# Kernel tuning notes

Hardware: AMD Instinct MI355X
Metric: run time of the kernel (lower is better)

The kernel has to match this reference:

```python
import jax, jax.numpy as jnp
import numpy as np

B, S, E = 4, 2048, 1024

def setup_inputs() -> dict:
    key = jax.random.key(0)
    ks = jax.random.split(key, 9)
    lim = 1.0 / np.sqrt(E)
    inp = {
        "query": jax.random.normal(ks[0], (B, S, E), dtype=jnp.float32),
        "key": jax.random.normal(ks[1], (B, S, E), dtype=jnp.float32),
        "value": jax.random.normal(ks[2], (B, S, E), dtype=jnp.float32),
        "Wq": jax.random.uniform(ks[3], (E, E), jnp.float32, -lim, lim),
        "bq": jax.random.uniform(ks[4], (E,), jnp.float32, -lim, lim),
        "Wk": jax.random.uniform(ks[5], (E, E), jnp.float32, -lim, lim),
        "bk": jax.random.uniform(ks[6], (E,), jnp.float32, -lim, lim),
        "Wv": jax.random.uniform(ks[7], (E, E), jnp.float32, -lim, lim),
        "bv": jax.random.uniform(ks[8], (E,), jnp.float32, -lim, lim),
    }
    return inp

def reference(query, key, value, Wq, bq, Wk, bk, Wv, bv):
    # Linear layers (torch stores weight as [out,in]; here W is [in,out] used as x @ W)
    q = query @ Wq + bq            # [B,S,E]
    k = key @ Wk + bk              # [B,S,E]
    v = value @ Wv + bv            # [B,S,E]
    inv_scale = jnp.asarray(E, q.dtype) ** 0.5
    scores = jnp.einsum("bse,bte->bst", q, k) / inv_scale  # [B,S,S]
    attn = jax.nn.softmax(scores, axis=-1)
    # dropout_p = 0.0 -> identity
    out = jnp.einsum("bst,bte->bse", attn, v)  # [B,S,E]
    return out
```

## Files before the change

### kernel.cpp

```cpp
#include <hip/hip_runtime.h>
#include <hip/hip_bf16.h>


typedef __bf16 bf16_t;
typedef bf16_t bf16x8 __attribute__((ext_vector_type(8)));
typedef bf16_t bf16x4 __attribute__((ext_vector_type(4)));
typedef float  f32x4  __attribute__((ext_vector_type(4)));

typedef const __attribute__((address_space(1))) unsigned gl_uint;
typedef __attribute__((address_space(3))) unsigned lds_uint;

#define BM 128
#define BN 128
#define BK 64

__device__ __forceinline__ void gload_lds16(const bf16_t* g, bf16_t* l) {
  __builtin_amdgcn_global_load_lds((gl_uint*)g, (lds_uint*)l, 16, 0, 0);
}

__device__ __forceinline__ void gemm_core(
    const bf16_t* __restrict__ Ab, const bf16_t* __restrict__ Bb,
    const int K, bf16_t* As, bf16_t* Bs, f32x4 acc[4][4])
{
  const int tid  = threadIdx.x;
  const int lane = tid & 63;
  const int quad = lane >> 4;
  const int l15  = lane & 15;
  const int wid  = tid >> 6;
  const int wm   = (wid >> 1) * 64;
  const int wn   = (wid & 1) * 64;
  const int csw  = l15 & 7;

  for (int kt = 0; kt < K; kt += BK) {
#pragma unroll
    for (int j = 0; j < 4; ++j) {
      const int lin = j * 256 + tid;
      const int row = lin >> 3;
      const int seg = (lin & 7) ^ (row & 7);
      gload_lds16(Ab + (size_t)row * K + kt + seg * 8, &As[lin * 8]);
    }
#pragma unroll
    for (int j = 0; j < 4; ++j) {
      const int lin = j * 256 + tid;
      const int row = lin >> 3;
      const int seg = (lin & 7) ^ (row & 7);
      gload_lds16(Bb + (size_t)row * K + kt + seg * 8, &Bs[lin * 8]);
    }
    __syncthreads();

#pragma unroll
    for (int ks = 0; ks < 2; ++ks) {
      const int sg = ks * 4 + quad;
      const int c  = (sg ^ csw) * 8;
      bf16x8 fa[4], fb[4];
#pragma unroll
      for (int i = 0; i < 4; ++i)
        fa[i] = *(const bf16x8*)&As[(wm + i * 16 + l15) * BK + c];
#pragma unroll
      for (int i = 0; i < 4; ++i)
        fb[i] = *(const bf16x8*)&Bs[(wn + i * 16 + l15) * BK + c];
#pragma unroll
      for (int mi = 0; mi < 4; ++mi)
#pragma unroll
        for (int ni = 0; ni < 4; ++ni)
          acc[mi][ni] = __builtin_amdgcn_mfma_f32_16x16x32_bf16(
              fa[mi], fb[ni], acc[mi][ni], 0, 0, 0);
    }
    __syncthreads();
  }
}

__global__ __launch_bounds__(256, 2)
void qkv_proj(const bf16_t* __restrict__ qb, const bf16_t* __restrict__ kb,
              const bf16_t* __restrict__ vb, const bf16_t* __restrict__ Wqt,
              const bf16_t* __restrict__ Wkt, const bf16_t* __restrict__ Wvt,
              const float* __restrict__ bq, const float* __restrict__ bk,
              const float* __restrict__ bv, bf16_t* __restrict__ qp,
              bf16_t* __restrict__ kp, bf16_t* __restrict__ vT)
{
  __shared__ __align__(16) bf16_t As[BM * BK];
  __shared__ __align__(16) bf16_t Bs[BN * BK];
  const int z = blockIdx.z;
  const bf16_t* A = (z == 0) ? qb : (z == 1) ? kb : vb;
  const bf16_t* W = (z == 0) ? Wqt : (z == 1) ? Wkt : Wvt;
  const float* bias = (z == 0) ? bq : (z == 1) ? bk : bv;

  const int K = 1024, N = 1024;
  const bf16_t* Ab = A + (size_t)blockIdx.y * BM * K;
  const bf16_t* Bb = W + (size_t)blockIdx.x * BN * K;

  f32x4 acc[4][4];
  const f32x4 z4 = {0.f, 0.f, 0.f, 0.f};
#pragma unroll
  for (int i = 0; i < 4; ++i)
#pragma unroll
    for (int j = 0; j < 4; ++j) acc[i][j] = z4;

  gemm_core(Ab, Bb, K, As, Bs, acc);

  const int lane = threadIdx.x & 63;
  const int quad = lane >> 4;
  const int l15  = lane & 15;
  const int wid  = threadIdx.x >> 6;
  const int wm = (wid >> 1) * 64, wn = (wid & 1) * 64;
  const int m0 = blockIdx.y * BM, n0 = blockIdx.x * BN;

#pragma unroll
  for (int mi = 0; mi < 4; ++mi) {
#pragma unroll
    for (int ni = 0; ni < 4; ++ni) {
      const int gn = n0 + wn + ni * 16 + l15;
      const int gm = m0 + wm + mi * 16 + quad * 4;
      const float bv_ = bias[gn];
      f32x4 a = acc[mi][ni];
      if (z < 2) {
        bf16_t* C = (z == 0) ? qp : kp;
#pragma unroll
        for (int r = 0; r < 4; ++r)
          C[(size_t)(gm + r) * N + gn] = (bf16_t)(a[r] + bv_);
      } else {
        const int b = gm >> 11;
        const int s = gm & 2047;
        bf16x4 o;
#pragma unroll
        for (int r = 0; r < 4; ++r) o[r] = (bf16_t)(a[r] + bv_);
        *(bf16x4*)&vT[((size_t)b * N + gn) * 2048 + s] = o;
      }
    }
  }
}

template <int MODE>
__global__ __launch_bounds__(256, 2)
void gemm_att(const bf16_t* __restrict__ A, const bf16_t* __restrict__ Bt,
              void* __restrict__ Cv, float* __restrict__ lsum,
              const int M, const int N, const int K,
              const long long sA, const long long sB, const long long sC)
{
  __shared__ __align__(16) bf16_t As[BM * BK];
  __shared__ __align__(16) bf16_t Bs[BN * BK];
  const int bz = blockIdx.z;
  const bf16_t* Ab = A + (size_t)bz * sA + (size_t)blockIdx.y * BM * K;
  const bf16_t* Bb = Bt + (size_t)bz * sB + (size_t)blockIdx.x * BN * K;

  f32x4 acc[4][4];
  const f32x4 z4 = {0.f, 0.f, 0.f, 0.f};
#pragma unroll
  for (int i = 0; i < 4; ++i)
#pragma unroll
    for (int j = 0; j < 4; ++j) acc[i][j] = z4;

  gemm_core(Ab, Bb, K, As, Bs, acc);

  const int lane = threadIdx.x & 63;
  const int quad = lane >> 4;
  const int l15  = lane & 15;
  const int wid  = threadIdx.x >> 6;
  const int wm = (wid >> 1) * 64, wn = (wid & 1) * 64;
  const int m0 = blockIdx.y * BM, n0 = blockIdx.x * BN;

  if (MODE == 0) {
    const float cexp = 0.03125f * 1.4426950408889634f;
    bf16_t* C = (bf16_t*)Cv + (size_t)bz * sC;
    float* lrow = lsum + (size_t)bz * M;
#pragma unroll
    for (int mi = 0; mi < 4; ++mi) {
      const int gm = m0 + wm + mi * 16 + quad * 4;
      float ps[4] = {0.f, 0.f, 0.f, 0.f};
#pragma unroll
      for (int ni = 0; ni < 4; ++ni) {
        const int gn = n0 + wn + ni * 16 + l15;
        f32x4 a = acc[mi][ni];
        float e[4];
#pragma unroll
        for (int r = 0; r < 4; ++r) {
          e[r] = exp2f(a[r] * cexp);
          C[(size_t)(gm + r) * N + gn] = (bf16_t)e[r];
          ps[r] += e[r];
        }
      }
#pragma unroll
      for (int o = 1; o <= 8; o <<= 1)
#pragma unroll
        for (int r = 0; r < 4; ++r) ps[r] += __shfl_xor(ps[r], o);
      if (l15 == 0) {
#pragma unroll
        for (int r = 0; r < 4; ++r) atomicAdd(&lrow[gm + r], ps[r]);
      }
    }
  } else {
    float* C = (float*)Cv + (size_t)bz * sC;
    const float* lrow = lsum + (size_t)bz * M;
#pragma unroll
    for (int mi = 0; mi < 4; ++mi) {
      const int gm = m0 + wm + mi * 16 + quad * 4;
      float il[4];
#pragma unroll
      for (int r = 0; r < 4; ++r) il[r] = 1.0f / lrow[gm + r];
#pragma unroll
      for (int ni = 0; ni < 4; ++ni) {
        const int gn = n0 + wn + ni * 16 + l15;
        f32x4 a = acc[mi][ni];
#pragma unroll
        for (int r = 0; r < 4; ++r)
          C[(size_t)(gm + r) * N + gn] = a[r] * il[r];
      }
    }
  }
}

__global__ __launch_bounds__(256)
void cvt3_k(const float* __restrict__ q, const float* __restrict__ k,
            const float* __restrict__ v, bf16_t* __restrict__ qo,
            bf16_t* __restrict__ ko, bf16_t* __restrict__ vo) {
  const int z = blockIdx.y;
  const float* in = (z == 0) ? q : (z == 1) ? k : v;
  bf16_t* out = (z == 0) ? qo : (z == 1) ? ko : vo;
  const size_t i = ((size_t)blockIdx.x * 256 + threadIdx.x) * 4;
  const float4 w = *(const float4*)(in + i);
  bf16x4 o;
  o[0] = (bf16_t)w.x; o[1] = (bf16_t)w.y; o[2] = (bf16_t)w.z; o[3] = (bf16_t)w.w;
  *(bf16x4*)(out + i) = o;
}

__global__ __launch_bounds__(256)
void transpose_cvt3(const float* __restrict__ Wq, const float* __restrict__ Wk,
                    const float* __restrict__ Wv, bf16_t* __restrict__ Wqt,
                    bf16_t* __restrict__ Wkt, bf16_t* __restrict__ Wvt) {
  const int z = blockIdx.z;
  const float* W = (z == 0) ? Wq : (z == 1) ? Wk : Wv;
  bf16_t* Wt = (z == 0) ? Wqt : (z == 1) ? Wkt : Wvt;
  __shared__ float tile[64][65];
  const int n0 = blockIdx.x * 64;
  const int k0 = blockIdx.y * 64;
  const int tid = threadIdx.x;
#pragma unroll
  for (int it = 0; it < 16; ++it) {
    const int idx = it * 256 + tid;
    const int r = idx >> 6, c = idx & 63;
    tile[r][c] = W[(size_t)(k0 + r) * 1024 + n0 + c];
  }
  __syncthreads();
#pragma unroll
  for (int it = 0; it < 16; ++it) {
    const int idx = it * 256 + tid;
    const int r = idx >> 6, c = idx & 63;
    Wt[(size_t)(n0 + r) * 1024 + k0 + c] = (bf16_t)tile[c][r];
  }
}

extern "C" void kernel_launch(void* const* d_in, const int* in_sizes, int n_in,
                              void* d_out, int out_size, void* d_ws, size_t ws_size,
                              hipStream_t stream) {
  const int B = 4, S = 2048, E = 1024;
  const size_t BSE = (size_t)B * S * E;
  const size_t EE  = (size_t)E * E;

  const float* q_in = (const float*)d_in[0];
  const float* k_in = (const float*)d_in[1];
  const float* v_in = (const float*)d_in[2];
  const float* Wq = (const float*)d_in[3];
  const float* bq = (const float*)d_in[4];
  const float* Wk = (const float*)d_in[5];
  const float* bk = (const float*)d_in[6];
  const float* Wv = (const float*)d_in[7];
  const float* bv = (const float*)d_in[8];
  float* out = (float*)d_out;

  char* ws = (char*)d_ws;
  bf16_t* qb  = (bf16_t*)ws;
  bf16_t* kb  = qb + BSE;
  bf16_t* vb  = kb + BSE;
  bf16_t* Wqt = vb + BSE;
  bf16_t* Wkt = Wqt + EE;
  bf16_t* Wvt = Wkt + EE;
  bf16_t* qp  = Wvt + EE;
  bf16_t* kp  = qp + BSE;
  bf16_t* vT  = kp + BSE;
  bf16_t* P   = vT + BSE;
  float*  lsum = (float*)(P + (size_t)B * S * S);

  cvt3_k<<<dim3(BSE / 1024, 3), 256, 0, stream>>>(q_in, k_in, v_in, qb, kb, vb);
  transpose_cvt3<<<dim3(16, 16, 3), 256, 0, stream>>>(Wq, Wk, Wv, Wqt, Wkt, Wvt);
  hipMemsetAsync(lsum, 0, (size_t)B * S * sizeof(float), stream);

  qkv_proj<<<dim3(E / BN, (B * S) / BM, 3), 256, 0, stream>>>(
      qb, kb, vb, Wqt, Wkt, Wvt, bq, bk, bv, qp, kp, vT);

  gemm_att<0><<<dim3(S / BN, S / BM, B), 256, 0, stream>>>(
      qp, kp, P, lsum, S, S, E,
      (long long)S * E, (long long)S * E, (long long)S * S);

  gemm_att<1><<<dim3(E / BN, S / BM, B), 256, 0, stream>>>(
      P, vT, out, lsum, S, E, S,
      (long long)S * S, (long long)E * S, (long long)S * E);

  (void)in_sizes; (void)n_in; (void)out_size; (void)ws_size;
}
```

Baseline: 319.6 us.

## Fuse fp32-to-bf16 input conversion into QKV GEMM and remap blocks per XCD

Removes the separate cvt3 kernel: qkv_proj now loads fp32 activations straight into LDS with swizzled global_load_lds and converts to bf16 while building MFMA fragments. All three GEMM kernels also switch to a 1D grid with a block index remap that groups tiles sharing A/B rows onto the same XCD (L&7) to improve L2 reuse. This saves a full read/write pass over the activations, but doubles LDS for the A tile (fp32) and adds conversion ALU work inside the inner loop, which may lower occupancy.

```diff
diff --git a/kernel.cpp b/kernel.cpp
--- a/kernel.cpp
+++ b/kernel.cpp
@@ -14,11 +14,11 @@
 #define BN 128
 #define BK 64
 
-__device__ __forceinline__ void gload_lds16(const bf16_t* g, bf16_t* l) {
+__device__ __forceinline__ void gload_lds16(const void* g, void* l) {
   __builtin_amdgcn_global_load_lds((gl_uint*)g, (lds_uint*)l, 16, 0, 0);
 }
 
-__device__ __forceinline__ void gemm_core(
+__device__ __forceinline__ void gemm_core_bf16(
     const bf16_t* __restrict__ Ab, const bf16_t* __restrict__ Bb,
     const int K, bf16_t* As, bf16_t* Bs, f32x4 acc[4][4])
 {
@@ -71,23 +71,40 @@
 }
 
 __global__ __launch_bounds__(256, 2)
-void qkv_proj(const bf16_t* __restrict__ qb, const bf16_t* __restrict__ kb,
-              const bf16_t* __restrict__ vb, const bf16_t* __restrict__ Wqt,
+void qkv_proj(const float* __restrict__ q, const float* __restrict__ k,
+              const float* __restrict__ v, const bf16_t* __restrict__ Wqt,
               const bf16_t* __restrict__ Wkt, const bf16_t* __restrict__ Wvt,
               const float* __restrict__ bq, const float* __restrict__ bk,
               const float* __restrict__ bv, bf16_t* __restrict__ qp,
               bf16_t* __restrict__ kp, bf16_t* __restrict__ vT)
 {
-  __shared__ __align__(16) bf16_t As[BM * BK];
+  __shared__ __align__(16) float  Asf[BM * BK];
   __shared__ __align__(16) bf16_t Bs[BN * BK];
-  const int z = blockIdx.z;
-  const bf16_t* A = (z == 0) ? qb : (z == 1) ? kb : vb;
-  const bf16_t* W = (z == 0) ? Wqt : (z == 1) ? Wkt : Wvt;
-  const float* bias = (z == 0) ? bq : (z == 1) ? bk : bv;
-
+
+  const int L = blockIdx.x;
+  const int g = L >> 3;
+  const int gst = (L & 7) * 3 + (g >> 6);
+  const int z  = gst >> 3;
+  const int sy = gst & 7;
+  const int w  = g & 63;
+  const int bx = w & 7;
+  const int by = sy * 8 + (w >> 3);
+
+  const float*  A    = (z == 0) ? q : (z == 1) ? k : v;
+  const bf16_t* W    = (z == 0) ? Wqt : (z == 1) ? Wkt : Wvt;
+  const float*  bias = (z == 0) ? bq : (z == 1) ? bk : bv;
   const int K = 1024, N = 1024;
-  const bf16_t* Ab = A + (size_t)blockIdx.y * BM * K;
-  const bf16_t* Bb = W + (size_t)blockIdx.x * BN * K;
+  const float*  Ab = A + (size_t)by * BM * K;
+  const bf16_t* Bb = W + (size_t)bx * BN * K;
+
+  const int tid  = threadIdx.x;
+  const int lane = tid & 63;
+  const int quad = lane >> 4;
+  const int l15  = lane & 15;
+  const int wid  = tid >> 6;
+  const int wm   = (wid >> 1) * 64;
+  const int wn   = (wid & 1) * 64;
+  const int r7   = l15 & 7;
 
   f32x4 acc[4][4];
   const f32x4 z4 = {0.f, 0.f, 0.f, 0.f};
@@ -96,15 +113,52 @@
 #pragma unroll
     for (int j = 0; j < 4; ++j) acc[i][j] = z4;
 
-  gemm_core(Ab, Bb, K, As, Bs, acc);
-
-  const int lane = threadIdx.x & 63;
-  const int quad = lane >> 4;
-  const int l15  = lane & 15;
-  const int wid  = threadIdx.x >> 6;
-  const int wm = (wid >> 1) * 64, wn = (wid & 1) * 64;
-  const int m0 = blockIdx.y * BM, n0 = blockIdx.x * BN;
-
+  for (int kt = 0; kt < K; kt += BK) {
+#pragma unroll
+    for (int j = 0; j < 8; ++j) {
+      const int lin = j * 256 + tid;
+      const int row = lin >> 4;
+      const int seg = (lin & 15) ^ (row & 7);
+      gload_lds16(Ab + (size_t)row * K + kt + seg * 4, &Asf[lin * 4]);
+    }
+#pragma unroll
+    for (int j = 0; j < 4; ++j) {
+      const int lin = j * 256 + tid;
+      const int row = lin >> 3;
+      const int seg = (lin & 7) ^ (row & 7);
+      gload_lds16(Bb + (size_t)row * K + kt + seg * 8, &Bs[lin * 8]);
+    }
+    __syncthreads();
+
+#pragma unroll
+    for (int ks = 0; ks < 2; ++ks) {
+      const int s0 = ks * 8 + quad * 2;
+      bf16x8 fa[4], fb[4];
+#pragma unroll
+      for (int i = 0; i < 4; ++i) {
+        const int row = wm + i * 16 + l15;
+        const f32x4 a0 = *(const f32x4*)&Asf[row * BK + ((s0)     ^ r7) * 4];
+        const f32x4 a1 = *(const f32x4*)&Asf[row * BK + ((s0 + 1) ^ r7) * 4];
+        bf16x8 f;
+#pragma unroll
+        for (int t = 0; t < 4; ++t) { f[t] = (bf16_t)a0[t]; f[4 + t] = (bf16_t)a1[t]; }
+        fa[i] = f;
+      }
+      const int cb = ((ks * 4 + quad) ^ r7) * 8;
+#pragma unroll
+      for (int i = 0; i < 4; ++i)
+        fb[i] = *(const bf16x8*)&Bs[(wn + i * 16 + l15) * BK + cb];
+#pragma unroll
+      for (int mi = 0; mi < 4; ++mi)
+#pragma unroll
+        for (int ni = 0; ni < 4; ++ni)
+          acc[mi][ni] = __builtin_amdgcn_mfma_f32_16x16x32_bf16(
+              fa[mi], fb[ni], acc[mi][ni], 0, 0, 0);
+    }
+    __syncthreads();
+  }
+
+  const int m0 = by * BM, n0 = bx * BN;
 #pragma unroll
   for (int mi = 0; mi < 4; ++mi) {
 #pragma unroll
@@ -139,9 +193,27 @@
 {
   __shared__ __align__(16) bf16_t As[BM * BK];
   __shared__ __align__(16) bf16_t Bs[BN * BK];
-  const int bz = blockIdx.z;
-  const bf16_t* Ab = A + (size_t)bz * sA + (size_t)blockIdx.y * BM * K;
-  const bf16_t* Bb = Bt + (size_t)bz * sB + (size_t)blockIdx.x * BN * K;
+
+  const int L = blockIdx.x;
+  int bx, by, bz;
+  if (MODE == 0) {
+    const int g = L >> 3;
+    const int gst = (L & 7) * 2 + (g >> 6);
+    bz = gst >> 2;
+    const int s2 = gst & 3;
+    const int w = g & 63;
+    bx = (s2 & 1) * 8 + (w & 7);
+    by = (s2 >> 1) * 8 + (w >> 3);
+  } else {
+    const int xcd = L & 7;
+    const int w = (L >> 3) & 63;
+    bz = xcd >> 1;
+    bx = w & 7;
+    by = (xcd & 1) * 8 + (w >> 3);
+  }
+
+  const bf16_t* Ab = A + (size_t)bz * sA + (size_t)by * BM * K;
+  const bf16_t* Bb = Bt + (size_t)bz * sB + (size_t)bx * BN * K;
 
   f32x4 acc[4][4];
   const f32x4 z4 = {0.f, 0.f, 0.f, 0.f};
@@ -150,14 +222,14 @@
 #pragma unroll
     for (int j = 0; j < 4; ++j) acc[i][j] = z4;
 
-  gemm_core(Ab, Bb, K, As, Bs, acc);
+  gemm_core_bf16(Ab, Bb, K, As, Bs, acc);
 
   const int lane = threadIdx.x & 63;
   const int quad = lane >> 4;
   const int l15  = lane & 15;
   const int wid  = threadIdx.x >> 6;
   const int wm = (wid >> 1) * 64, wn = (wid & 1) * 64;
-  const int m0 = blockIdx.y * BM, n0 = blockIdx.x * BN;
+  const int m0 = by * BM, n0 = bx * BN;
 
   if (MODE == 0) {
     const float cexp = 0.03125f * 1.4426950408889634f;
@@ -171,12 +243,11 @@
       for (int ni = 0; ni < 4; ++ni) {
         const int gn = n0 + wn + ni * 16 + l15;
         f32x4 a = acc[mi][ni];
-        float e[4];
 #pragma unroll
         for (int r = 0; r < 4; ++r) {
-          e[r] = exp2f(a[r] * cexp);
-          C[(size_t)(gm + r) * N + gn] = (bf16_t)e[r];
-          ps[r] += e[r];
+          const float e = exp2f(a[r] * cexp);
+          C[(size_t)(gm + r) * N + gn] = (bf16_t)e;
+          ps[r] += e;
         }
       }
 #pragma unroll
@@ -207,20 +278,6 @@
       }
     }
   }
-}
-
-__global__ __launch_bounds__(256)
-void cvt3_k(const float* __restrict__ q, const float* __restrict__ k,
-            const float* __restrict__ v, bf16_t* __restrict__ qo,
-            bf16_t* __restrict__ ko, bf16_t* __restrict__ vo) {
-  const int z = blockIdx.y;
-  const float* in = (z == 0) ? q : (z == 1) ? k : v;
-  bf16_t* out = (z == 0) ? qo : (z == 1) ? ko : vo;
-  const size_t i = ((size_t)blockIdx.x * 256 + threadIdx.x) * 4;
-  const float4 w = *(const float4*)(in + i);
-  bf16x4 o;
-  o[0] = (bf16_t)w.x; o[1] = (bf16_t)w.y; o[2] = (bf16_t)w.z; o[3] = (bf16_t)w.w;
-  *(bf16x4*)(out + i) = o;
 }
 
 __global__ __launch_bounds__(256)
@@ -268,10 +325,7 @@
   float* out = (float*)d_out;
 
   char* ws = (char*)d_ws;
-  bf16_t* qb  = (bf16_t*)ws;
-  bf16_t* kb  = qb + BSE;
-  bf16_t* vb  = kb + BSE;
-  bf16_t* Wqt = vb + BSE;
+  bf16_t* Wqt = (bf16_t*)ws;
   bf16_t* Wkt = Wqt + EE;
   bf16_t* Wvt = Wkt + EE;
   bf16_t* qp  = Wvt + EE;
@@ -280,18 +334,17 @@
   bf16_t* P   = vT + BSE;
   float*  lsum = (float*)(P + (size_t)B * S * S);
 
-  cvt3_k<<<dim3(BSE / 1024, 3), 256, 0, stream>>>(q_in, k_in, v_in, qb, kb, vb);
   transpose_cvt3<<<dim3(16, 16, 3), 256, 0, stream>>>(Wq, Wk, Wv, Wqt, Wkt, Wvt);
   hipMemsetAsync(lsum, 0, (size_t)B * S * sizeof(float), stream);
 
-  qkv_proj<<<dim3(E / BN, (B * S) / BM, 3), 256, 0, stream>>>(
-      qb, kb, vb, Wqt, Wkt, Wvt, bq, bk, bv, qp, kp, vT);
-
-  gemm_att<0><<<dim3(S / BN, S / BM, B), 256, 0, stream>>>(
+  qkv_proj<<<1536, 256, 0, stream>>>(q_in, k_in, v_in, Wqt, Wkt, Wvt,
+                                     bq, bk, bv, qp, kp, vT);
+
+  gemm_att<0><<<1024, 256, 0, stream>>>(
       qp, kp, P, lsum, S, S, E,
       (long long)S * E, (long long)S * E, (long long)S * S);
 
-  gemm_att<1><<<dim3(E / BN, S / BM, B), 256, 0, stream>>>(
+  gemm_att<1><<<512, 256, 0, stream>>>(
       P, vT, out, lsum, S, E, S,
       (long long)S * S, (long long)E * S, (long long)S * E);
 
```

After: 303.1 us. 1.05x faster.
